# Kernel tuning notes

Measured on AMD Instinct MI355X. Metric: run time of the kernel, lower is better.

Reference implementation:

```python
import jax, jax.numpy as jnp
import numpy as np

TEMPERATURE = 0.1
NEG_INF = -1e9
EPS = 1e-12

def setup_inputs() -> dict:
    key = jax.random.key(0)
    k1, k2, k3 = jax.random.split(key, 3)
    B, C, H, W = 8, 256, 128, 128
    num_classes = 150
    features = jax.random.normal(k1, (B, C, H, W), dtype=jnp.float32)
    labels = jax.random.randint(k2, (B, H, W), 0, num_classes, dtype=jnp.int32)
    text_embeddings = jax.random.normal(k3, (num_classes, C), dtype=jnp.float32)
    return {"features": features, "labels": labels, "text_embeddings": text_embeddings, "ignore_index": 255}

def _l2_normalize(x, axis=-1):
    n = jnp.linalg.norm(x, axis=axis, keepdims=True)
    return x / jnp.maximum(n, EPS)

def reference(features, labels, text_embeddings, ignore_index):
    num_classes, C = text_embeddings.shape
    B = features.shape[0]
    # [B,C,H,W] -> [B*H*W, C]
    f = jnp.transpose(features, (0, 2, 3, 1)).reshape(-1, C)
    lab = jnp.where(labels == ignore_index, 0, labels).reshape(-1)
    # segment-mean per class (fused scatter-add instead of per-class loop)
    sums = jax.ops.segment_sum(f, lab, num_segments=num_classes)          # [K,C]
    counts = jax.ops.segment_sum(jnp.ones_like(lab, dtype=f.dtype), lab, num_segments=num_classes)  # [K]
    valid = counts > 0
    prototypes = jnp.where(valid[:, None], sums / jnp.maximum(counts, 1.0)[:, None], 0.0)
    prototypes = _l2_normalize(prototypes)
    text_n = _l2_normalize(text_embeddings)
    sim = (prototypes @ text_n.T) / TEMPERATURE                            # [K,K]
    # cross-entropy restricted to valid rows/cols with identity soft targets
    masked = jnp.where(valid[None, :], sim, NEG_INF)                       # mask invalid cols
    logp = jax.nn.log_softmax(masked, axis=-1)
    diag = jnp.diagonal(logp)
    per_row = jnp.where(valid, -diag, 0.0)
    n_valid = jnp.sum(valid.astype(f.dtype))
    loss = jnp.sum(per_row) / jnp.maximum(n_valid, 1.0)
    return jnp.where(n_valid > 1, loss, 0.0)
```

## Files before the change

kernel.cpp:

```cpp
#include <hip/hip_runtime.h>
#include <math.h>

#define EPSV 1e-12f

typedef __attribute__((ext_vector_type(8))) short short8;
typedef __attribute__((ext_vector_type(4))) float f32x4;

constexpr int MT    = 10;
constexpr int K_PAD = MT * 16;
constexpr int PBPX  = 512;
constexpr int NKS   = PBPX / 32;
constexpr int NPB   = 256;
constexpr int THR   = 512;

__global__ __launch_bounds__(THR, 4) void protomm_kernel(
    const float* __restrict__ feat,
    const int*   __restrict__ labels,
    const int*   __restrict__ ign_p,
    float*       __restrict__ partial,
    float*       __restrict__ vmask,
    int C, int HW)
{
    __shared__ int   labL[PBPX];
    __shared__ float ftile[16][132];
    __shared__ unsigned char pres[K_PAD];

    const int tid   = threadIdx.x;
    const int ct    = tid >> 6;
    const int l     = tid & 63;
    const int rowid = l & 15;
    const int g     = l >> 4;

    const int bid = blockIdx.x;
    const int cg  = bid & 1;
    const int pb  = bid >> 1;
    const int b   = pb >> 5;
    const int px0 = (pb & 31) * PBPX;
    const int ig  = *ign_p;

    if (cg == 0)
        for (int i = tid; i < K_PAD; i += THR) pres[i] = 0;
    {
        int lv = labels[(size_t)b * HW + px0 + tid];
        labL[tid] = (lv == ig) ? 0 : lv;
    }
    __syncthreads();
    if (cg == 0) {
        int lv = labL[tid];
        if ((unsigned)lv < (unsigned)K_PAD) pres[lv] = 1;
    }

    const float* bbase = feat
        + ((size_t)(b * C + cg * 128 + ct * 16 + rowid)) * HW + px0 + g * 8;

    f32x4 acc[MT];
    #pragma unroll
    for (int m = 0; m < MT; ++m) acc[m] = (f32x4){0.f, 0.f, 0.f, 0.f};

    float4 xa0, xa1, xb0, xb1;
    auto LOADA = [&](int ks) {
        const float* p = bbase + ks * 32;
        xa0 = *reinterpret_cast<const float4*>(p);
        xa1 = *reinterpret_cast<const float4*>(p + 4);
    };
    auto LOADB = [&](int ks) {
        const float* p = bbase + ks * 32;
        xb0 = *reinterpret_cast<const float4*>(p);
        xb1 = *reinterpret_cast<const float4*>(p + 4);
    };
    auto CONSUME = [&](int ks, float4 x0, float4 x1) {
        unsigned w0, w1, w2, w3;
        asm("v_cvt_pk_bf16_f32 %0, %1, %2" : "=v"(w0) : "v"(x0.x), "v"(x0.y));
        asm("v_cvt_pk_bf16_f32 %0, %1, %2" : "=v"(w1) : "v"(x0.z), "v"(x0.w));
        asm("v_cvt_pk_bf16_f32 %0, %1, %2" : "=v"(w2) : "v"(x1.x), "v"(x1.y));
        asm("v_cvt_pk_bf16_f32 %0, %1, %2" : "=v"(w3) : "v"(x1.z), "v"(x1.w));
        uint4 bw = make_uint4(w0, w1, w2, w3);
        short8 bfrag = __builtin_bit_cast(short8, bw);
        const int4 lA = *reinterpret_cast<const int4*>(&labL[ks * 32 + g * 8]);
        const int4 lB = *reinterpret_cast<const int4*>(&labL[ks * 32 + g * 8 + 4]);
        #pragma unroll
        for (int m = 0; m < MT; ++m) {
            const int tgt = m * 16 + rowid;
            unsigned a0 = (lA.x == tgt ? 0x3F80u : 0u) | (lA.y == tgt ? 0x3F800000u : 0u);
            unsigned a1 = (lA.z == tgt ? 0x3F80u : 0u) | (lA.w == tgt ? 0x3F800000u : 0u);
            unsigned a2 = (lB.x == tgt ? 0x3F80u : 0u) | (lB.y == tgt ? 0x3F800000u : 0u);
            unsigned a3 = (lB.z == tgt ? 0x3F80u : 0u) | (lB.w == tgt ? 0x3F800000u : 0u);
            uint4 aw = make_uint4(a0, a1, a2, a3);
            short8 afrag = __builtin_bit_cast(short8, aw);
            acc[m] = __builtin_amdgcn_mfma_f32_16x16x32_bf16(afrag, bfrag, acc[m], 0, 0, 0);
        }
    };

    LOADA(0);
    LOADB(1);
    #pragma unroll 1
    for (int ks = 0; ks < NKS; ks += 2) {
        CONSUME(ks, xa0, xa1);
        if (ks + 2 < NKS) LOADA(ks + 2);
        CONSUME(ks + 1, xb0, xb1);
        if (ks + 3 < NKS) LOADB(ks + 3);
    }

    __syncthreads();
    #pragma unroll
    for (int m = 0; m < MT; ++m) {
        #pragma unroll
        for (int r = 0; r < 4; ++r)
            ftile[g * 4 + r][ct * 16 + rowid] = acc[m][r];
        __syncthreads();
        {
            const int row = tid >> 5, cq = tid & 31;
            float4 v = *reinterpret_cast<const float4*>(&ftile[row][4 * cq]);
            *reinterpret_cast<float4*>(
                partial + (size_t)pb * K_PAD * C + (size_t)(m * 16 + row) * C
                        + cg * 128 + 4 * cq) = v;
        }
        __syncthreads();
    }

    if (cg == 0)
        for (int i = tid; i < K_PAD; i += THR)
            if (pres[i]) vmask[i] = 1.0f;
}

__global__ __launch_bounds__(256) void tail_kernel(
    const float* __restrict__ partial,
    const float* __restrict__ text,
    const float* __restrict__ vmask,
    float* __restrict__ loss_acc,
    unsigned int* __restrict__ ticket,
    float* __restrict__ out,
    int K, int C, int nblocks)
{
    __shared__ float ph[256];
    __shared__ float scr[4][260];
    __shared__ float vm[K_PAD];
    __shared__ float red[5];
    __shared__ float wred[12];
    __shared__ unsigned int lastflag;

    const int k    = blockIdx.x;
    const int tid  = threadIdx.x;
    const int wid  = tid >> 6;
    const int lane = tid & 63;

    if (tid < K_PAD) vm[tid] = vmask[tid];
    __syncthreads();
    const bool valid = (vm[k] > 0.f);

    float contrib = 0.f;
    if (valid) {
        const int cq = tid & 63;
        const int sg = tid >> 6;
        const size_t gs = (size_t)K_PAD * C;
        const float* pbase = partial + (size_t)k * C + 4 * cq;
        float4 a0 = {0,0,0,0}, a1 = {0,0,0,0}, a2 = {0,0,0,0}, a3 = {0,0,0,0};
        float4 a4 = {0,0,0,0}, a5 = {0,0,0,0}, a6 = {0,0,0,0}, a7 = {0,0,0,0};
        for (int o = 0; o < NPB; o += 32) {
            a0 += *(const float4*)(pbase + (size_t)(o + sg +  0) * gs);
            a1 += *(const float4*)(pbase + (size_t)(o + sg +  4) * gs);
            a2 += *(const float4*)(pbase + (size_t)(o + sg +  8) * gs);
            a3 += *(const float4*)(pbase + (size_t)(o + sg + 12) * gs);
            a4 += *(const float4*)(pbase + (size_t)(o + sg + 16) * gs);
            a5 += *(const float4*)(pbase + (size_t)(o + sg + 20) * gs);
            a6 += *(const float4*)(pbase + (size_t)(o + sg + 24) * gs);
            a7 += *(const float4*)(pbase + (size_t)(o + sg + 28) * gs);
        }
        float4 asum = (((a0 + a1) + (a2 + a3)) + ((a4 + a5) + (a6 + a7)));
        *(float4*)&scr[sg][4 * cq] = asum;
        __syncthreads();
        float val = scr[0][tid] + scr[1][tid] + scr[2][tid] + scr[3][tid];

        float v = val * val;
        #pragma unroll
        for (int o = 32; o > 0; o >>= 1) v += __shfl_down(v, o);
        if (lane == 0) red[wid] = v;
        __syncthreads();
        if (tid == 0) {
            float s = red[0] + red[1] + red[2] + red[3];
            red[4] = 1.0f / fmaxf(sqrtf(s), EPSV);
        }
        __syncthreads();
        ph[tid] = val * red[4];
        __syncthreads();

        const float4 pv = *(const float4*)&ph[4 * lane];
        float m = -INFINITY, s = 0.f, skk = 0.f;
        #pragma unroll 1
        for (int gq = 0; gq < K_PAD / 16; ++gq) {
            const int j0 = gq * 16 + wid * 4;
            const float4* t0 = (const float4*)(text + (size_t)(j0 + 0 < K ? j0 + 0 : 0) * C);
            const float4* t1 = (const float4*)(text + (size_t)(j0 + 1 < K ? j0 + 1 : 0) * C);
            const float4* t2 = (const float4*)(text + (size_t)(j0 + 2 < K ? j0 + 2 : 0) * C);
            const float4* t3 = (const float4*)(text + (size_t)(j0 + 3 < K ? j0 + 3 : 0) * C);
            float4 x0 = t0[lane], x1 = t1[lane], x2 = t2[lane], x3 = t3[lane];
            float d0 = pv.x*x0.x + pv.y*x0.y + pv.z*x0.z + pv.w*x0.w;
            float q0 = x0.x*x0.x + x0.y*x0.y + x0.z*x0.z + x0.w*x0.w;
            float d1 = pv.x*x1.x + pv.y*x1.y + pv.z*x1.z + pv.w*x1.w;
            float q1 = x1.x*x1.x + x1.y*x1.y + x1.z*x1.z + x1.w*x1.w;
            float d2 = pv.x*x2.x + pv.y*x2.y + pv.z*x2.z + pv.w*x2.w;
            float q2 = x2.x*x2.x + x2.y*x2.y + x2.z*x2.z + x2.w*x2.w;
            float d3 = pv.x*x3.x + pv.y*x3.y + pv.z*x3.z + pv.w*x3.w;
            float q3 = x3.x*x3.x + x3.y*x3.y + x3.z*x3.z + x3.w*x3.w;
            #pragma unroll
            for (int o = 32; o > 0; o >>= 1) {
                d0 += __shfl_down(d0, o); d1 += __shfl_down(d1, o);
                d2 += __shfl_down(d2, o); d3 += __shfl_down(d3, o);
                q0 += __shfl_down(q0, o); q1 += __shfl_down(q1, o);
                q2 += __shfl_down(q2, o); q3 += __shfl_down(q3, o);
            }
            if (lane == 0) {
                float dd[4] = {d0, d1, d2, d3};
                float qq[4] = {q0, q1, q2, q3};
                #pragma unroll
                for (int r = 0; r < 4; ++r) {
                    int j = j0 + r;
                    float vmj = vm[j];
                    float sim = dd[r] * (10.0f / fmaxf(sqrtf(qq[r]), EPSV));
                    float ms  = vmj * sim - (1.f - vmj) * 1e9f;
                    if (j == k) skk = ms;
                    if (ms > m) { s = s * __expf(m - ms) + 1.f; m = ms; }
                    else        { s += __expf(ms - m); }
                }
            }
        }
        if (lane == 0) { wred[wid*3+0] = m; wred[wid*3+1] = s; wred[wid*3+2] = skk; }
        __syncthreads();
        if (tid == 0) {
            float M = fmaxf(fmaxf(wred[0], wred[3]), fmaxf(wred[6], wred[9]));
            float S = 0.f, SKK = 0.f;
            #pragma unroll
            for (int ww = 0; ww < 4; ++ww) {
                S   += wred[ww*3+1] * __expf(wred[ww*3+0] - M);
                SKK += wred[ww*3+2];
            }
            contrib = M + logf(S) - SKK;
        }
    }

    if (tid == 0) {
        if (valid) atomicAdd(loss_acc, contrib);
        __threadfence();
        unsigned old = atomicAdd(ticket, 1u);
        lastflag = (old == (unsigned)(nblocks - 1)) ? 1u : 0u;
    }
    __syncthreads();
    if (lastflag) {
        float v = (tid < K_PAD) ? vm[tid] : 0.f;
        #pragma unroll
        for (int o = 32; o > 0; o >>= 1) v += __shfl_down(v, o);
        if (lane == 0) red[wid] = v;
        __syncthreads();
        if (tid == 0) {
            float nv = red[0] + red[1] + red[2] + red[3];
            float total = atomicAdd(loss_acc, 0.0f);
            out[0] = (nv > 1.f) ? total / fmaxf(nv, 1.f) : 0.f;
        }
    }
}

extern "C" void kernel_launch(void* const* d_in, const int* in_sizes, int n_in,
                              void* d_out, int out_size, void* d_ws, size_t ws_size,
                              hipStream_t stream) {
    const float* feat   = (const float*)d_in[0];
    const int*   labels = (const int*)d_in[1];
    const float* text   = (const float*)d_in[2];
    const int*   ign    = (const int*)d_in[3];

    const int B  = 8;
    const int N  = in_sizes[1];
    const int HW = N / B;
    const int C  = in_sizes[0] / N;
    const int K  = in_sizes[2] / C;

    float*        partial  = (float*)d_ws;
    float*        vmask    = partial + (size_t)NPB * K_PAD * C;
    float*        loss_acc = vmask + K_PAD;
    unsigned int* ticket   = (unsigned int*)(loss_acc + 1);

    hipMemsetAsync(vmask, 0, (K_PAD + 2) * sizeof(float), stream);

    protomm_kernel<<<NPB * 2, THR, 0, stream>>>(
        feat, labels, ign, partial, vmask, C, HW);

    tail_kernel<<<K, 256, 0, stream>>>(
        partial, text, vmask, loss_acc, ticket, (float*)d_out, K, C, K);
}
```

Measured before the change: 80.80 us.

## Stage bf16 feature tiles in LDS and split class tiles across waves

Restructures the one-hot segment-sum GEMM. Each block now covers 1024 pixels and 32 channels, giving 8 channel groups and 128 pixel blocks. Features are loaded coalesced along pixels, converted to bf16 and double-buffered in shared memory. Each wave pair owns a 16-channel slice and computes only 3 of the 10 class tiles, which cuts registers per thread and allows a higher launch-bounds occupancy. In exchange it adds block-wide barriers per chunk and leaves some waves idle, since 10 class tiles do not divide evenly across 4 parities.

After: 85.39 us. 5.7% more time.

```diff
diff --git a/kernel.cpp b/kernel.cpp
--- a/kernel.cpp
+++ b/kernel.cpp
@@ -8,12 +8,16 @@
 
 constexpr int MT    = 10;
 constexpr int K_PAD = MT * 16;
-constexpr int PBPX  = 512;
-constexpr int NKS   = PBPX / 32;
-constexpr int NPB   = 256;
+constexpr int CPB   = 32;
+constexpr int CG    = 8;
+constexpr int CHUNK = 128;
+constexpr int PBPX  = 1024;
+constexpr int NCHK  = PBPX / CHUNK;
+constexpr int NPB   = 128;
 constexpr int THR   = 512;
-
-__global__ __launch_bounds__(THR, 4) void protomm_kernel(
+constexpr int LROW  = 136;
+
+__global__ __launch_bounds__(THR, 8) void protomm_kernel(
     const float* __restrict__ feat,
     const int*   __restrict__ labels,
     const int*   __restrict__ ign_p,
@@ -21,99 +25,128 @@
     float*       __restrict__ vmask,
     int C, int HW)
 {
+    __shared__ unsigned short Bf[2][CPB * LROW];
     __shared__ int   labL[PBPX];
-    __shared__ float ftile[16][132];
+    __shared__ float ftile[4][16][36];
     __shared__ unsigned char pres[K_PAD];
 
     const int tid   = threadIdx.x;
-    const int ct    = tid >> 6;
+    const int w     = tid >> 6;
     const int l     = tid & 63;
+    const int ct    = w & 1;
+    const int par   = w >> 1;
     const int rowid = l & 15;
     const int g     = l >> 4;
 
     const int bid = blockIdx.x;
-    const int cg  = bid & 1;
-    const int pb  = bid >> 1;
-    const int b   = pb >> 5;
-    const int px0 = (pb & 31) * PBPX;
+    const int cg  = bid & 7;
+    const int pb  = bid >> 3;
+    const int b   = pb >> 4;
+    const int px0 = (pb & 15) * PBPX;
     const int ig  = *ign_p;
+
+    const int qq  = tid & 31;
+    const int chp = tid >> 5;
+    const float* fb = feat + ((size_t)(b * C + cg * CPB + chp)) * HW + px0 + 4 * qq;
+    const int*   lb = labels + (size_t)b * HW + px0;
 
     if (cg == 0)
         for (int i = tid; i < K_PAD; i += THR) pres[i] = 0;
-    {
-        int lv = labels[(size_t)b * HW + px0 + tid];
-        labL[tid] = (lv == ig) ? 0 : lv;
+    #pragma unroll
+    for (int i = 0; i < PBPX / THR; ++i) {
+        int lv = lb[tid + i * THR];
+        labL[tid + i * THR] = (lv == ig) ? 0 : lv;
     }
     __syncthreads();
     if (cg == 0) {
-        int lv = labL[tid];
-        if ((unsigned)lv < (unsigned)K_PAD) pres[lv] = 1;
-    }
-
-    const float* bbase = feat
-        + ((size_t)(b * C + cg * 128 + ct * 16 + rowid)) * HW + px0 + g * 8;
-
-    f32x4 acc[MT];
+        #pragma unroll
+        for (int i = 0; i < PBPX / THR; ++i) {
+            int la = labL[tid + i * THR];
+            if ((unsigned)la < (unsigned)K_PAD) pres[la] = 1;
+        }
+    }
+
+    f32x4 acc[3];
     #pragma unroll
-    for (int m = 0; m < MT; ++m) acc[m] = (f32x4){0.f, 0.f, 0.f, 0.f};
+    for (int j = 0; j < 3; ++j) acc[j] = (f32x4){0.f, 0.f, 0.f, 0.f};
 
     float4 xa0, xa1, xb0, xb1;
-    auto LOADA = [&](int ks) {
-        const float* p = bbase + ks * 32;
+    auto issueA = [&](int ck) {
+        const float* p = fb + ck * CHUNK;
         xa0 = *reinterpret_cast<const float4*>(p);
-        xa1 = *reinterpret_cast<const float4*>(p + 4);
+        xa1 = *reinterpret_cast<const float4*>(p + (size_t)16 * HW);
     };
-    auto LOADB = [&](int ks) {
-        const float* p = bbase + ks * 32;
+    auto issueB = [&](int ck) {
+        const float* p = fb + ck * CHUNK;
         xb0 = *reinterpret_cast<const float4*>(p);
-        xb1 = *reinterpret_cast<const float4*>(p + 4);
+        xb1 = *reinterpret_cast<const float4*>(p + (size_t)16 * HW);
     };
-    auto CONSUME = [&](int ks, float4 x0, float4 x1) {
-        unsigned w0, w1, w2, w3;
-        asm("v_cvt_pk_bf16_f32 %0, %1, %2" : "=v"(w0) : "v"(x0.x), "v"(x0.y));
-        asm("v_cvt_pk_bf16_f32 %0, %1, %2" : "=v"(w1) : "v"(x0.z), "v"(x0.w));
-        asm("v_cvt_pk_bf16_f32 %0, %1, %2" : "=v"(w2) : "v"(x1.x), "v"(x1.y));
-        asm("v_cvt_pk_bf16_f32 %0, %1, %2" : "=v"(w3) : "v"(x1.z), "v"(x1.w));
-        uint4 bw = make_uint4(w0, w1, w2, w3);
-        short8 bfrag = __builtin_bit_cast(short8, bw);
-        const int4 lA = *reinterpret_cast<const int4*>(&labL[ks * 32 + g * 8]);
-        const int4 lB = *reinterpret_cast<const int4*>(&labL[ks * 32 + g * 8 + 4]);
+    auto commit = [&](int buf, float4 v0, float4 v1) {
+        unsigned p0, p1, p2, p3;
+        asm("v_cvt_pk_bf16_f32 %0, %1, %2" : "=v"(p0) : "v"(v0.x), "v"(v0.y));
+        asm("v_cvt_pk_bf16_f32 %0, %1, %2" : "=v"(p1) : "v"(v0.z), "v"(v0.w));
+        asm("v_cvt_pk_bf16_f32 %0, %1, %2" : "=v"(p2) : "v"(v1.x), "v"(v1.y));
+        asm("v_cvt_pk_bf16_f32 %0, %1, %2" : "=v"(p3) : "v"(v1.z), "v"(v1.w));
+        *reinterpret_cast<uint2*>(&Bf[buf][chp * LROW + 4 * qq])        = make_uint2(p0, p1);
+        *reinterpret_cast<uint2*>(&Bf[buf][(chp + 16) * LROW + 4 * qq]) = make_uint2(p2, p3);
+    };
+    auto CONSUME = [&](int buf, int ck) {
         #pragma unroll
-        for (int m = 0; m < MT; ++m) {
-            const int tgt = m * 16 + rowid;
-            unsigned a0 = (lA.x == tgt ? 0x3F80u : 0u) | (lA.y == tgt ? 0x3F800000u : 0u);
-            unsigned a1 = (lA.z == tgt ? 0x3F80u : 0u) | (lA.w == tgt ? 0x3F800000u : 0u);
-            unsigned a2 = (lB.x == tgt ? 0x3F80u : 0u) | (lB.y == tgt ? 0x3F800000u : 0u);
-            unsigned a3 = (lB.z == tgt ? 0x3F80u : 0u) | (lB.w == tgt ? 0x3F800000u : 0u);
-            uint4 aw = make_uint4(a0, a1, a2, a3);
-            short8 afrag = __builtin_bit_cast(short8, aw);
-            acc[m] = __builtin_amdgcn_mfma_f32_16x16x32_bf16(afrag, bfrag, acc[m], 0, 0, 0);
+        for (int ks = 0; ks < 4; ++ks) {
+            const int4 lA = *reinterpret_cast<const int4*>(&labL[ck * CHUNK + ks * 32 + g * 8]);
+            const int4 lB = *reinterpret_cast<const int4*>(&labL[ck * CHUNK + ks * 32 + g * 8 + 4]);
+            const short8 bfrag = *reinterpret_cast<const short8*>(
+                &Bf[buf][(ct * 16 + rowid) * LROW + ks * 32 + g * 8]);
+            #pragma unroll
+            for (int j = 0; j < 3; ++j) {
+                const int m = par + 4 * j;
+                if (m < MT) {
+                    const int tgt = m * 16 + rowid;
+                    unsigned a0 = (lA.x == tgt ? 0x3F80u : 0u) | (lA.y == tgt ? 0x3F800000u : 0u);
+                    unsigned a1 = (lA.z == tgt ? 0x3F80u : 0u) | (lA.w == tgt ? 0x3F800000u : 0u);
+                    unsigned a2 = (lB.x == tgt ? 0x3F80u : 0u) | (lB.y == tgt ? 0x3F800000u : 0u);
+                    unsigned a3 = (lB.z == tgt ? 0x3F80u : 0u) | (lB.w == tgt ? 0x3F800000u : 0u);
+                    uint4 aw = make_uint4(a0, a1, a2, a3);
+                    short8 afrag = __builtin_bit_cast(short8, aw);
+                    acc[j] = __builtin_amdgcn_mfma_f32_16x16x32_bf16(afrag, bfrag, acc[j], 0, 0, 0);
+                }
+            }
         }
     };
 
-    LOADA(0);
-    LOADB(1);
+    issueA(0);
     #pragma unroll 1
-    for (int ks = 0; ks < NKS; ks += 2) {
-        CONSUME(ks, xa0, xa1);
-        if (ks + 2 < NKS) LOADA(ks + 2);
-        CONSUME(ks + 1, xb0, xb1);
-        if (ks + 3 < NKS) LOADB(ks + 3);
+    for (int it = 0; it < NCHK / 2; ++it) {
+        const int ck = 2 * it;
+        issueB(ck + 1);
+        commit(0, xa0, xa1);
+        __syncthreads();
+        CONSUME(0, ck);
+        if (ck + 2 < NCHK) issueA(ck + 2);
+        commit(1, xb0, xb1);
+        __syncthreads();
+        CONSUME(1, ck + 1);
     }
 
     __syncthreads();
-    #pragma unroll
-    for (int m = 0; m < MT; ++m) {
-        #pragma unroll
-        for (int r = 0; r < 4; ++r)
-            ftile[g * 4 + r][ct * 16 + rowid] = acc[m][r];
+    #pragma unroll 1
+    for (int j = 0; j < 3; ++j) {
+        const int m = par + 4 * j;
+        if (m < MT) {
+            #pragma unroll
+            for (int r = 0; r < 4; ++r)
+                ftile[par][g * 4 + r][ct * 16 + rowid] = acc[j][r];
+        }
         __syncthreads();
         {
-            const int row = tid >> 5, cq = tid & 31;
-            float4 v = *reinterpret_cast<const float4*>(&ftile[row][4 * cq]);
-            *reinterpret_cast<float4*>(
-                partial + (size_t)pb * K_PAD * C + (size_t)(m * 16 + row) * C
-                        + cg * 128 + 4 * cq) = v;
+            const int par2 = tid >> 7, row = (tid >> 3) & 15, cq = tid & 7;
+            const int m2 = par2 + 4 * j;
+            if (m2 < MT) {
+                float4 v = *reinterpret_cast<const float4*>(&ftile[par2][row][4 * cq]);
+                *reinterpret_cast<float4*>(
+                    partial + (size_t)pb * K_PAD * C + (size_t)(m2 * 16 + row) * C
+                            + cg * CPB + 4 * cq) = v;
+            }
         }
         __syncthreads();
     }
@@ -280,7 +313,7 @@
 
     hipMemsetAsync(vmask, 0, (K_PAD + 2) * sizeof(float), stream);
 
-    protomm_kernel<<<NPB * 2, THR, 0, stream>>>(
+    protomm_kernel<<<NPB * CG, THR, 0, stream>>>(
         feat, labels, ign, partial, vmask, C, HW);
 
     tail_kernel<<<K, 256, 0, stream>>>(
```

## Stage feature tiles through LDS with async global_load_lds quad-buffered pipeline

Applied to the files above, without the earlier changes.

Replaces direct per-thread global float4 loads with async global_load_lds into a 4-deep swizzled LDS ring, with explicit vmcnt waits and barriers. The work split also changes: each block now covers 64 channels over 1024 pixels and gets 4 channel groups, and each warp owns a subset of class tiles for two channel subtiles. Fewer pixel blocks (128) halve the partial-sum buffer the tail kernel reduces. Partials are written straight from registers without the LDS transpose. The risk is higher LDS use (64KB+), which lowers occupancy, plus uncoalesced scattered partial stores.

Result: faster. 71.38 us (-11.7%).

```diff
diff --git a/kernel.cpp b/kernel.cpp
--- a/kernel.cpp
+++ b/kernel.cpp
@@ -7,10 +7,12 @@
 typedef __attribute__((ext_vector_type(4))) float f32x4;
 
 constexpr int MT    = 10;
-constexpr int K_PAD = MT * 16;
-constexpr int PBPX  = 512;
-constexpr int NKS   = PBPX / 32;
-constexpr int NPB   = 256;
+constexpr int K_PAD = 160;
+constexpr int CPB   = 64;
+constexpr int CHPX  = 64;
+constexpr int PBPX  = 1024;
+constexpr int NCHK  = PBPX / CHPX;
+constexpr int NPB   = 128;
 constexpr int THR   = 512;
 
 __global__ __launch_bounds__(THR, 4) void protomm_kernel(
@@ -21,106 +23,161 @@
     float*       __restrict__ vmask,
     int C, int HW)
 {
+    __shared__ float stage[4][4096];
     __shared__ int   labL[PBPX];
-    __shared__ float ftile[16][132];
     __shared__ unsigned char pres[K_PAD];
 
     const int tid   = threadIdx.x;
-    const int ct    = tid >> 6;
-    const int l     = tid & 63;
-    const int rowid = l & 15;
-    const int g     = l >> 4;
+    const int w     = tid >> 6;
+    const int lane  = tid & 63;
+    const int rowid = lane & 15;
+    const int g     = lane >> 4;
+    const int ctg   = w & 1;
+    const int mg    = w >> 1;
 
     const int bid = blockIdx.x;
-    const int cg  = bid & 1;
-    const int pb  = bid >> 1;
-    const int b   = pb >> 5;
-    const int px0 = (pb & 31) * PBPX;
+    const int cg  = bid & 3;
+    const int pb  = bid >> 2;
+    const int b   = pb >> 4;
+    const int px0 = (pb & 15) * PBPX;
     const int ig  = *ign_p;
 
     if (cg == 0)
         for (int i = tid; i < K_PAD; i += THR) pres[i] = 0;
     {
-        int lv = labels[(size_t)b * HW + px0 + tid];
-        labL[tid] = (lv == ig) ? 0 : lv;
+        int l0 = labels[(size_t)b * HW + px0 + tid];
+        int l1 = labels[(size_t)b * HW + px0 + THR + tid];
+        labL[tid]       = (l0 == ig) ? 0 : l0;
+        labL[tid + THR] = (l1 == ig) ? 0 : l1;
     }
     __syncthreads();
     if (cg == 0) {
-        int lv = labL[tid];
-        if ((unsigned)lv < (unsigned)K_PAD) pres[lv] = 1;
-    }
-
-    const float* bbase = feat
-        + ((size_t)(b * C + cg * 128 + ct * 16 + rowid)) * HW + px0 + g * 8;
-
-    f32x4 acc[MT];
+        int la = labL[tid];
+        if ((unsigned)la < (unsigned)K_PAD) pres[la] = 1;
+        la = labL[tid + THR];
+        if ((unsigned)la < (unsigned)K_PAD) pres[la] = 1;
+    }
+
+    const int sch = tid >> 4;
+    const int p40 = (tid & 15) ^ (sch & 7);
+    const float* gb0 = feat + ((size_t)(b * C + cg * CPB + sch)) * HW + px0 + 4 * p40;
+    const float* gb1 = gb0 + (size_t)32 * HW;
+
+    auto ISSUE = [&](int ck) {
+        const int buf = ck & 3;
+        __builtin_amdgcn_global_load_lds(
+            (const __attribute__((address_space(1))) void*)(gb0 + ck * CHPX),
+            (__attribute__((address_space(3))) void*)&stage[buf][tid * 4], 16, 0, 0);
+        __builtin_amdgcn_global_load_lds(
+            (const __attribute__((address_space(1))) void*)(gb1 + ck * CHPX),
+            (__attribute__((address_space(3))) void*)&stage[buf][tid * 4 + 2048], 16, 0, 0);
+    };
+
+    f32x4 acc0[3], acc1[3];
     #pragma unroll
-    for (int m = 0; m < MT; ++m) acc[m] = (f32x4){0.f, 0.f, 0.f, 0.f};
-
-    float4 xa0, xa1, xb0, xb1;
-    auto LOADA = [&](int ks) {
-        const float* p = bbase + ks * 32;
-        xa0 = *reinterpret_cast<const float4*>(p);
-        xa1 = *reinterpret_cast<const float4*>(p + 4);
+    for (int j = 0; j < 3; ++j) {
+        acc0[j] = (f32x4){0.f, 0.f, 0.f, 0.f};
+        acc1[j] = (f32x4){0.f, 0.f, 0.f, 0.f};
+    }
+
+    auto CONSUME = [&](int ck) {
+        const int buf = ck & 3;
+        #pragma unroll
+        for (int ks = 0; ks < 2; ++ks) {
+            const int pxb = ck * CHPX + ks * 32 + g * 8;
+            const int4 lA = *reinterpret_cast<const int4*>(&labL[pxb]);
+            const int4 lB = *reinterpret_cast<const int4*>(&labL[pxb + 4]);
+            const int px4 = ks * 8 + g * 2;
+            short8 bfr0, bfr1;
+            {
+                const int ch = ctg * 32 + rowid;
+                const int x  = ch & 7;
+                const float4 f0 = *reinterpret_cast<const float4*>(
+                    &stage[buf][(ch * 16 + (px4 ^ x)) * 4]);
+                const float4 f1 = *reinterpret_cast<const float4*>(
+                    &stage[buf][(ch * 16 + ((px4 + 1) ^ x)) * 4]);
+                unsigned q0, q1, q2, q3;
+                asm("v_cvt_pk_bf16_f32 %0, %1, %2" : "=v"(q0) : "v"(f0.x), "v"(f0.y));
+                asm("v_cvt_pk_bf16_f32 %0, %1, %2" : "=v"(q1) : "v"(f0.z), "v"(f0.w));
+                asm("v_cvt_pk_bf16_f32 %0, %1, %2" : "=v"(q2) : "v"(f1.x), "v"(f1.y));
+                asm("v_cvt_pk_bf16_f32 %0, %1, %2" : "=v"(q3) : "v"(f1.z), "v"(f1.w));
+                bfr0 = __builtin_bit_cast(short8, make_uint4(q0, q1, q2, q3));
+            }
+            {
+                const int ch = ctg * 32 + 16 + rowid;
+                const int x  = ch & 7;
+                const float4 f0 = *reinterpret_cast<const float4*>(
+                    &stage[buf][(ch * 16 + (px4 ^ x)) * 4]);
+                const float4 f1 = *reinterpret_cast<const float4*>(
+                    &stage[buf][(ch * 16 + ((px4 + 1) ^ x)) * 4]);
+                unsigned q0, q1, q2, q3;
+                asm("v_cvt_pk_bf16_f32 %0, %1, %2" : "=v"(q0) : "v"(f0.x), "v"(f0.y));
+                asm("v_cvt_pk_bf16_f32 %0, %1, %2" : "=v"(q1) : "v"(f0.z), "v"(f0.w));
+                asm("v_cvt_pk_bf16_f32 %0, %1, %2" : "=v"(q2) : "v"(f1.x), "v"(f1.y));
+                asm("v_cvt_pk_bf16_f32 %0, %1, %2" : "=v"(q3) : "v"(f1.z), "v"(f1.w));
+                bfr1 = __builtin_bit_cast(short8, make_uint4(q0, q1, q2, q3));
+            }
+            #pragma unroll
+            for (int j = 0; j < 3; ++j) {
+                const int m = mg + 4 * j;
+                if (m < MT) {
+                    const int tgt = m * 16 + rowid;
+                    unsigned a0 = (lA.x == tgt ? 0x3F80u : 0u) | (lA.y == tgt ? 0x3F800000u : 0u);
+                    unsigned a1 = (lA.z == tgt ? 0x3F80u : 0u) | (lA.w == tgt ? 0x3F800000u : 0u);
+                    unsigned a2 = (lB.x == tgt ? 0x3F80u : 0u) | (lB.y == tgt ? 0x3F800000u : 0u);
+                    unsigned a3 = (lB.z == tgt ? 0x3F80u : 0u) | (lB.w == tgt ? 0x3F800000u : 0u);
+                    short8 afrag = __builtin_bit_cast(short8, make_uint4(a0, a1, a2, a3));
+                    acc0[j] = __builtin_amdgcn_mfma_f32_16x16x32_bf16(afrag, bfr0, acc0[j], 0, 0, 0);
+                    acc1[j] = __builtin_amdgcn_mfma_f32_16x16x32_bf16(afrag, bfr1, acc1[j], 0, 0, 0);
+                }
+            }
+        }
     };
-    auto LOADB = [&](int ks) {
-        const float* p = bbase + ks * 32;
-        xb0 = *reinterpret_cast<const float4*>(p);
-        xb1 = *reinterpret_cast<const float4*>(p + 4);
-    };
-    auto CONSUME = [&](int ks, float4 x0, float4 x1) {
-        unsigned w0, w1, w2, w3;
-        asm("v_cvt_pk_bf16_f32 %0, %1, %2" : "=v"(w0) : "v"(x0.x), "v"(x0.y));
-        asm("v_cvt_pk_bf16_f32 %0, %1, %2" : "=v"(w1) : "v"(x0.z), "v"(x0.w));
-        asm("v_cvt_pk_bf16_f32 %0, %1, %2" : "=v"(w2) : "v"(x1.x), "v"(x1.y));
-        asm("v_cvt_pk_bf16_f32 %0, %1, %2" : "=v"(w3) : "v"(x1.z), "v"(x1.w));
-        uint4 bw = make_uint4(w0, w1, w2, w3);
-        short8 bfrag = __builtin_bit_cast(short8, bw);
-        const int4 lA = *reinterpret_cast<const int4*>(&labL[ks * 32 + g * 8]);
-        const int4 lB = *reinterpret_cast<const int4*>(&labL[ks * 32 + g * 8 + 4]);
+
+    ISSUE(0); ISSUE(1); ISSUE(2);
+    #pragma unroll 1
+    for (int ck = 0; ck < NCHK - 2; ++ck) {
+        asm volatile("s_waitcnt vmcnt(4)" ::: "memory");
+        __builtin_amdgcn_sched_barrier(0);
+        __builtin_amdgcn_s_barrier();
+        __builtin_amdgcn_sched_barrier(0);
+        if (ck + 3 < NCHK) ISSUE(ck + 3);
+        CONSUME(ck);
+    }
+    asm volatile("s_waitcnt vmcnt(2)" ::: "memory");
+    __builtin_amdgcn_sched_barrier(0);
+    __builtin_amdgcn_s_barrier();
+    __builtin_amdgcn_sched_barrier(0);
+    CONSUME(NCHK - 2);
+    asm volatile("s_waitcnt vmcnt(0)" ::: "memory");
+    __builtin_amdgcn_sched_barrier(0);
+    __builtin_amdgcn_s_barrier();
+    __builtin_amdgcn_sched_barrier(0);
+    CONSUME(NCHK - 1);
+
+    {
+        float* dst = partial + (size_t)pb * K_PAD * C + cg * CPB;
         #pragma unroll
-        for (int m = 0; m < MT; ++m) {
-            const int tgt = m * 16 + rowid;
-            unsigned a0 = (lA.x == tgt ? 0x3F80u : 0u) | (lA.y == tgt ? 0x3F800000u : 0u);
-            unsigned a1 = (lA.z == tgt ? 0x3F80u : 0u) | (lA.w == tgt ? 0x3F800000u : 0u);
-            unsigned a2 = (lB.x == tgt ? 0x3F80u : 0u) | (lB.y == tgt ? 0x3F800000u : 0u);
-            unsigned a3 = (lB.z == tgt ? 0x3F80u : 0u) | (lB.w == tgt ? 0x3F800000u : 0u);
-            uint4 aw = make_uint4(a0, a1, a2, a3);
-            short8 afrag = __builtin_bit_cast(short8, aw);
-            acc[m] = __builtin_amdgcn_mfma_f32_16x16x32_bf16(afrag, bfrag, acc[m], 0, 0, 0);
-        }
-    };
-
-    LOADA(0);
-    LOADB(1);
-    #pragma unroll 1
-    for (int ks = 0; ks < NKS; ks += 2) {
-        CONSUME(ks, xa0, xa1);
-        if (ks + 2 < NKS) LOADA(ks + 2);
-        CONSUME(ks + 1, xb0, xb1);
-        if (ks + 3 < NKS) LOADB(ks + 3);
-    }
-
-    __syncthreads();
-    #pragma unroll
-    for (int m = 0; m < MT; ++m) {
-        #pragma unroll
-        for (int r = 0; r < 4; ++r)
-            ftile[g * 4 + r][ct * 16 + rowid] = acc[m][r];
-        __syncthreads();
-        {
-            const int row = tid >> 5, cq = tid & 31;
-            float4 v = *reinterpret_cast<const float4*>(&ftile[row][4 * cq]);
-            *reinterpret_cast<float4*>(
-                partial + (size_t)pb * K_PAD * C + (size_t)(m * 16 + row) * C
-                        + cg * 128 + 4 * cq) = v;
-        }
-        __syncthreads();
-    }
-
-    if (cg == 0)
+        for (int j = 0; j < 3; ++j) {
+            const int m = mg + 4 * j;
+            if (m < MT) {
+                #pragma unroll
+                for (int c2 = 0; c2 < 2; ++c2) {
+                    const int col = (ctg * 2 + c2) * 16 + rowid;
+                    #pragma unroll
+                    for (int r = 0; r < 4; ++r) {
+                        const int cls = m * 16 + g * 4 + r;
+                        dst[(size_t)cls * C + col] = (c2 == 0) ? acc0[j][r] : acc1[j][r];
+                    }
+                }
+            }
+        }
+    }
+    if (cg == 0) {
+        __syncthreads();
         for (int i = tid; i < K_PAD; i += THR)
             if (pres[i]) vmask[i] = 1.0f;
+    }
 }
 
 __global__ __launch_bounds__(256) void tail_kernel(
@@ -280,7 +337,7 @@
 
     hipMemsetAsync(vmask, 0, (K_PAD + 2) * sizeof(float), stream);
 
-    protomm_kernel<<<NPB * 2, THR, 0, stream>>>(
+    protomm_kernel<<<NPB * 4, THR, 0, stream>>>(
         feat, labels, ign, partial, vmask, C, HW);
 
     tail_kernel<<<K, 256, 0, stream>>>(
```
